# Kernel tuning notes

Measured on AMD Instinct MI355X. Metric: run time of the kernel, lower is better.

Reference implementation:

```python
import jax, jax.numpy as jnp
import numpy as np

N = 100000
E = 1600000
IN_FEATS = 128
HIDDEN = 128
CLASSES = 64


def setup_inputs() -> dict:
    key = jax.random.key(0)
    ks = jax.random.split(key, 8)
    features = jax.random.normal(ks[0], (N, IN_FEATS), dtype=jnp.float32)
    edge_index = jax.random.randint(ks[1], (2, E), 0, N, dtype=jnp.int64 if jax.config.jax_enable_x64 else jnp.int32)
    # Glorot-init weights like PyG's GCNConv.lin, zero bias
    def glorot(k, fan_in, fan_out):
        lim = (6.0 / (fan_in + fan_out)) ** 0.5
        return jax.random.uniform(k, (fan_in, fan_out), dtype=jnp.float32, minval=-lim, maxval=lim)
    return {
        "features": features,
        "edge_index": edge_index,
        "W1": glorot(ks[2], IN_FEATS, HIDDEN), "b1": jnp.zeros((HIDDEN,), jnp.float32),
        "W2": glorot(ks[3], HIDDEN, HIDDEN), "b2": jnp.zeros((HIDDEN,), jnp.float32),
        "W3": glorot(ks[4], HIDDEN, CLASSES), "b3": jnp.zeros((CLASSES,), jnp.float32),
    }


def _gcn_conv(x, W, b, row, col, deg_norm_row, deg_norm_col):
    # x: [N, d_in] -> [N, d_out]. PyG GCNConv: linear first, then normalized aggregation, then bias.
    xw = x @ W                                   # [N, d_out]
    norm = deg_norm_row * deg_norm_col          # [E]
    msg = norm[:, None] * xw[row]               # gather from source nodes
    out = jax.ops.segment_sum(msg, col, num_segments=N)  # scatter-add to dst
    return out + b


def reference(features, edge_index, W1, b1, W2, b2, W3, b3):
    row, col = edge_index[0], edge_index[1]  # source -> target
    # gcn_norm with add_self_loops=False, unit edge weights: deg over dst nodes
    deg = jax.ops.segment_sum(jnp.ones((E,), features.dtype), col, num_segments=N)
    dinv = jnp.where(deg > 0, jax.lax.rsqrt(jnp.maximum(deg, 1.0)), 0.0)
    dn_row, dn_col = dinv[row], dinv[col]
    h = jax.nn.relu(_gcn_conv(features, W1, b1, row, col, dn_row, dn_col))
    h = jax.nn.relu(_gcn_conv(h, W2, b2, row, col, dn_row, dn_col))
    h = jax.nn.relu(_gcn_conv(h, W3, b3, row, col, dn_row, dn_col))
    return h
```

## Files before the change

kernel.cpp:

```cpp
#include <hip/hip_runtime.h>

#define ALIGNUP(x) (((x) + 255) & ~(size_t)255)
#define ABLK 256
#define BSHIFT 9

typedef _Float16 f16x8 __attribute__((ext_vector_type(8)));
typedef float f32x4 __attribute__((ext_vector_type(4)));


__global__ void bucket_hist_kernel(const int* __restrict__ col, unsigned* __restrict__ gHist,
                                   int nE, int chunk) {
    __shared__ unsigned hist[256];
    const int tid = threadIdx.x, blk = blockIdx.x;
    hist[tid] = 0;
    __syncthreads();
    const int e0 = blk * chunk, e1 = min(nE, e0 + chunk);
    for (int e = e0 + tid; e < e1; e += 256)
        atomicAdd(&hist[((unsigned)col[e]) >> BSHIFT], 1u);
    __syncthreads();
    gHist[tid * ABLK + blk] = hist[tid];
}

__global__ void bucket_scan_kernel(unsigned* __restrict__ g) {
    __shared__ unsigned ps[1024];
    const int tid = threadIdx.x;
    const int base = tid * 64;
    unsigned sum = 0;
    for (int k = 0; k < 64; ++k) sum += g[base + k];
    ps[tid] = sum;
    __syncthreads();
    for (int o = 1; o < 1024; o <<= 1) {
        unsigned t = tid >= o ? ps[tid - o] : 0u;
        __syncthreads();
        ps[tid] += t;
        __syncthreads();
    }
    unsigned run = ps[tid] - sum;
    for (int k = 0; k < 64; ++k) {
        unsigned v = g[base + k];
        g[base + k] = run;
        run += v;
    }
}

__global__ void bucket_scatter_kernel(const int* __restrict__ row, const int* __restrict__ col,
                                      const unsigned* __restrict__ gScan,
                                      unsigned* __restrict__ pairs, int nE, int chunk) {
    __shared__ unsigned basec[256];
    const int tid = threadIdx.x, blk = blockIdx.x;
    basec[tid] = gScan[tid * ABLK + blk];
    __syncthreads();
    const int e0 = blk * chunk, e1 = min(nE, e0 + chunk);
    for (int e = e0 + tid; e < e1; e += 256) {
        unsigned d = (unsigned)col[e];
        unsigned pos = atomicAdd(&basec[d >> BSHIFT], 1u);
        pairs[pos] = (((unsigned)row[e]) << BSHIFT) | (d & 511u);
    }
}

__global__ void bucket_sort_kernel(const unsigned* __restrict__ pairs,
                                   const unsigned* __restrict__ gScan,
                                   int* __restrict__ srcs, int* __restrict__ off,
                                   float* __restrict__ dinv, int nN, int nE) {
    __shared__ unsigned cnt[512], sc[512];
    const int tid = threadIdx.x, b = blockIdx.x;
    const unsigned s = gScan[b * ABLK];
    const unsigned t = (b + 1 < 256) ? gScan[(b + 1) * ABLK] : (unsigned)nE;
    cnt[tid] = 0;
    __syncthreads();
    for (unsigned i = s + tid; i < t; i += 512)
        atomicAdd(&cnt[pairs[i] & 511u], 1u);
    __syncthreads();
    const unsigned v = cnt[tid];
    sc[tid] = v;
    __syncthreads();
    for (int o = 1; o < 512; o <<= 1) {
        unsigned q = tid >= o ? sc[tid - o] : 0u;
        __syncthreads();
        sc[tid] += q;
        __syncthreads();
    }
    const unsigned excl = sc[tid] - v;
    const int node = b * 512 + tid;
    if (node < nN) {
        dinv[node] = v > 0 ? rsqrtf((float)v) : 0.f;
        off[node] = (int)(s + excl);
    }
    if (b == 0 && tid == 0) off[nN] = nE;
    sc[tid] = excl;
    __syncthreads();
    for (unsigned i = s + tid; i < t; i += 512) {
        unsigned p = pairs[i];
        unsigned pos = s + atomicAdd(&sc[p & 511u], 1u);
        srcs[pos] = (int)(p >> BSHIFT);
    }
}


template <int DOUT, bool AF32>
__launch_bounds__(256)
__global__ void gemm_mfma(const void* __restrict__ Xv, const float* __restrict__ W,
                          const float* __restrict__ dinv, _Float16* __restrict__ Y, int nrows) {
    constexpr int NTILE = DOUT / 16;
    __shared__ f16x8 Wf[NTILE * 4 * 64];
    const int tid = threadIdx.x;
    for (int idx = tid; idx < 128 * (DOUT / 4); idx += 256) {
        const int kk = idx / (DOUT / 4);
        const int n4 = (idx % (DOUT / 4)) * 4;
        const float4 w = ((const float4*)W)[idx];
        const int fk = kk >> 5, kb = (kk >> 3) & 3, e = kk & 7;
        const float wv[4] = {w.x, w.y, w.z, w.w};
#pragma unroll
        for (int d = 0; d < 4; ++d) {
            const int n = n4 + d;
            const int j = n >> 4;
            const int l = (n & 15) | (kb << 4);
            ((_Float16*)&Wf[(j * 4 + fk) * 64 + l])[e] = (_Float16)wv[d];
        }
    }
    __syncthreads();

    const int lane = tid & 63;
    const int wvid = tid >> 6;
    const int m = lane & 15;
    const int kb = lane >> 4;
    const int nchunks = (nrows + 63) >> 6;

    for (int c = blockIdx.x; c < nchunks; c += gridDim.x) {
        const int r0 = c * 64 + wvid * 16;
        const int arow = min(r0 + m, nrows - 1);
        f16x8 a[4];
        if constexpr (AF32) {
            const float* Xp = (const float*)Xv + (size_t)arow * 128 + kb * 8;
#pragma unroll
            for (int k = 0; k < 4; ++k) {
                const float4 x0 = *(const float4*)(Xp + k * 32);
                const float4 x1 = *(const float4*)(Xp + k * 32 + 4);
                f16x8 t;
                t[0] = (_Float16)x0.x; t[1] = (_Float16)x0.y;
                t[2] = (_Float16)x0.z; t[3] = (_Float16)x0.w;
                t[4] = (_Float16)x1.x; t[5] = (_Float16)x1.y;
                t[6] = (_Float16)x1.z; t[7] = (_Float16)x1.w;
                a[k] = t;
            }
        } else {
            const _Float16* Xp = (const _Float16*)Xv + (size_t)arow * 128 + kb * 8;
#pragma unroll
            for (int k = 0; k < 4; ++k) a[k] = *(const f16x8*)(Xp + k * 32);
        }
        f32x4 acc[NTILE];
#pragma unroll
        for (int j = 0; j < NTILE; ++j) acc[j] = (f32x4){0.f, 0.f, 0.f, 0.f};
#pragma unroll
        for (int k = 0; k < 4; ++k)
#pragma unroll
            for (int j = 0; j < NTILE; ++j)
                acc[j] = __builtin_amdgcn_mfma_f32_16x16x32_f16(
                             a[k], Wf[(j * 4 + k) * 64 + lane], acc[j], 0, 0, 0);
#pragma unroll
        for (int i = 0; i < 4; ++i) {
            const int r = r0 + kb * 4 + i;
            if (r < nrows) {
                const float dv = dinv[r];
#pragma unroll
                for (int j = 0; j < NTILE; ++j)
                    Y[(size_t)r * DOUT + j * 16 + m] = (_Float16)(acc[j][i] * dv);
            }
        }
    }
}


template <int D, typename OT>
__launch_bounds__(256)
__global__ void gather_kernel(const _Float16* __restrict__ XW, const int* __restrict__ off,
                              const int* __restrict__ srcs, const float* __restrict__ dinv,
                              const float* __restrict__ bias, OT* __restrict__ out, int nN) {
    constexpr int G   = D / 8;
    constexpr int EPW = 64 / G;
    const int lane = threadIdx.x & 63;
    const int g    = lane % G;
    const int sub  = lane / G;
    const int wid  = (blockIdx.x * blockDim.x + threadIdx.x) >> 6;
    const int nw   = (gridDim.x * blockDim.x) >> 6;

    for (int v = wid; v < nN; v += nw) {
        const int s1 = off[v + 1];
        int i = off[v] + sub;
        float acc[8];
#pragma unroll
        for (int k = 0; k < 8; ++k) acc[k] = 0.f;
        for (; i + EPW < s1; i += 2 * EPW) {
            int sa = srcs[i], sb = srcs[i + EPW];
            union { uint4 u; _Float16 h[8]; } ca, cb;
            ca.u = ((const uint4*)(XW + (size_t)sa * D))[g];
            cb.u = ((const uint4*)(XW + (size_t)sb * D))[g];
#pragma unroll
            for (int k = 0; k < 8; ++k) acc[k] += (float)ca.h[k];
#pragma unroll
            for (int k = 0; k < 8; ++k) acc[k] += (float)cb.h[k];
        }
        if (i < s1) {
            union { uint4 u; _Float16 h[8]; } cv;
            cv.u = ((const uint4*)(XW + (size_t)srcs[i] * D))[g];
#pragma unroll
            for (int k = 0; k < 8; ++k) acc[k] += (float)cv.h[k];
        }
#pragma unroll
        for (int d = 32; d >= G; d >>= 1)
#pragma unroll
            for (int k = 0; k < 8; ++k) acc[k] += __shfl_down(acc[k], d);
        if (sub == 0) {
            const float dv = dinv[v];
            const float4 b0 = ((const float4*)bias)[g * 2];
            const float4 b1 = ((const float4*)bias)[g * 2 + 1];
            float o[8];
            o[0] = fmaxf(dv * acc[0] + b0.x, 0.f);
            o[1] = fmaxf(dv * acc[1] + b0.y, 0.f);
            o[2] = fmaxf(dv * acc[2] + b0.z, 0.f);
            o[3] = fmaxf(dv * acc[3] + b0.w, 0.f);
            o[4] = fmaxf(dv * acc[4] + b1.x, 0.f);
            o[5] = fmaxf(dv * acc[5] + b1.y, 0.f);
            o[6] = fmaxf(dv * acc[6] + b1.z, 0.f);
            o[7] = fmaxf(dv * acc[7] + b1.w, 0.f);
            if constexpr (sizeof(OT) == 2) {
                union { uint4 u; _Float16 h[8]; } ov;
#pragma unroll
                for (int k = 0; k < 8; ++k) ov.h[k] = (_Float16)o[k];
                *(uint4*)((_Float16*)out + (size_t)v * D + g * 8) = ov.u;
            } else {
                float4 o0 = make_float4(o[0], o[1], o[2], o[3]);
                float4 o1 = make_float4(o[4], o[5], o[6], o[7]);
                float4* op = (float4*)((float*)out + (size_t)v * D + g * 8);
                op[0] = o0;
                op[1] = o1;
            }
        }
    }
}

extern "C" void kernel_launch(void* const* d_in, const int* in_sizes, int n_in,
                              void* d_out, int out_size, void* d_ws, size_t ws_size,
                              hipStream_t stream) {
    const float* feats = (const float*)d_in[0];
    const int*   ei    = (const int*)d_in[1];
    const float* W1    = (const float*)d_in[2];
    const float* b1    = (const float*)d_in[3];
    const float* W2    = (const float*)d_in[4];
    const float* b2    = (const float*)d_in[5];
    const float* W3    = (const float*)d_in[6];
    const float* b3    = (const float*)d_in[7];

    const int N = in_sizes[0] / 128;
    const int E = in_sizes[1] / 2;
    const int* row = ei;
    const int* col = ei + E;

    char* p = (char*)d_ws;
    unsigned* gHist = (unsigned*)p; p += ALIGNUP((size_t)256 * ABLK * 4);
    float*     dinv = (float*)p;    p += ALIGNUP((size_t)N * 4);
    int*       off  = (int*)p;      p += ALIGNUP((size_t)(N + 1) * 4);
    int*       srcs = (int*)p;      p += ALIGNUP((size_t)E * 4);
    _Float16*  bufW = (_Float16*)p; p += ALIGNUP((size_t)N * 128 * 2);
    _Float16*  bufX = (_Float16*)p;
    unsigned* pairs = (unsigned*)bufX;

    const int chunk = (E + ABLK - 1) / ABLK;
    const int NB    = (N + 511) >> BSHIFT;
    bucket_hist_kernel<<<ABLK, 256, 0, stream>>>(col, gHist, E, chunk);
    bucket_scan_kernel<<<1, 1024, 0, stream>>>(gHist);
    bucket_scatter_kernel<<<ABLK, 256, 0, stream>>>(row, col, gHist, pairs, E, chunk);
    bucket_sort_kernel<<<NB, 512, 0, stream>>>(pairs, gHist, srcs, off, dinv, N, E);

    const int NCH = (N + 63) / 64;
    const int GG  = NCH < 800 ? NCH : 800;
    const int GB  = (N + 3) / 4;

    gemm_mfma<128, true><<<GG, 256, 0, stream>>>(feats, W1, dinv, bufW, N);
    gather_kernel<128, _Float16><<<GB, 256, 0, stream>>>(bufW, off, srcs, dinv, b1, bufX, N);
    gemm_mfma<128, false><<<GG, 256, 0, stream>>>(bufX, W2, dinv, bufW, N);
    gather_kernel<128, _Float16><<<GB, 256, 0, stream>>>(bufW, off, srcs, dinv, b2, bufX, N);
    gemm_mfma<64, false><<<GG, 256, 0, stream>>>(bufX, W3, dinv, bufW, N);
    gather_kernel<64, float><<<GB, 256, 0, stream>>>(bufW, off, srcs, dinv, b3,
                                                     (float*)d_out, N);
}
```

Measured before the change: 299.8 us.

## Gather with one 8-lane group per node and split features into column halves

Replaces the wave-per-node gather with a kernel in which each wave handles eight nodes, one 8-lane group per node. Each group loads a batch of source indices cooperatively and broadcasts them with shuffles, so the cross-lane reduction goes away and work per node is finer-grained. The 128-wide layers are now aggregated in two passes over 64-column halves, shrinking the working set of each pass so more of it can stay in cache. The cost is reading the index lists twice per wide layer, launching more kernels, and load imbalance within a wave when node degrees differ.

```diff
diff --git a/kernel.cpp b/kernel.cpp
--- a/kernel.cpp
+++ b/kernel.cpp
@@ -171,49 +171,57 @@
 }
 
 
-template <int D, typename OT>
+template <int DW, int LD, typename OT>
 __launch_bounds__(256)
-__global__ void gather_kernel(const _Float16* __restrict__ XW, const int* __restrict__ off,
-                              const int* __restrict__ srcs, const float* __restrict__ dinv,
-                              const float* __restrict__ bias, OT* __restrict__ out, int nN) {
-    constexpr int G   = D / 8;
-    constexpr int EPW = 64 / G;
+__global__ void gather_grp(const _Float16* __restrict__ XW, const int* __restrict__ off,
+                           const int* __restrict__ srcs, const float* __restrict__ dinv,
+                           const float* __restrict__ bias, OT* __restrict__ out, int nN) {
+    constexpr int G   = DW / 8;
+    constexpr int GPW = 64 / G;
     const int lane = threadIdx.x & 63;
-    const int g    = lane % G;
-    const int sub  = lane / G;
+    const int gl   = lane % G;
+    const int grp  = lane / G;
     const int wid  = (blockIdx.x * blockDim.x + threadIdx.x) >> 6;
     const int nw   = (gridDim.x * blockDim.x) >> 6;
 
-    for (int v = wid; v < nN; v += nw) {
-        const int s1 = off[v + 1];
-        int i = off[v] + sub;
+    for (int v0 = wid * GPW; v0 < nN; v0 += nw * GPW) {
+        const int v   = v0 + grp;
+        const bool act = v < nN;
+        const int s0 = act ? off[v] : 0;
+        const int s1 = act ? off[v + 1] : 0;
         float acc[8];
 #pragma unroll
         for (int k = 0; k < 8; ++k) acc[k] = 0.f;
-        for (; i + EPW < s1; i += 2 * EPW) {
-            int sa = srcs[i], sb = srcs[i + EPW];
-            union { uint4 u; _Float16 h[8]; } ca, cb;
-            ca.u = ((const uint4*)(XW + (size_t)sa * D))[g];
-            cb.u = ((const uint4*)(XW + (size_t)sb * D))[g];
-#pragma unroll
-            for (int k = 0; k < 8; ++k) acc[k] += (float)ca.h[k];
-#pragma unroll
-            for (int k = 0; k < 8; ++k) acc[k] += (float)cb.h[k];
-        }
-        if (i < s1) {
-            union { uint4 u; _Float16 h[8]; } cv;
-            cv.u = ((const uint4*)(XW + (size_t)srcs[i] * D))[g];
-#pragma unroll
-            for (int k = 0; k < 8; ++k) acc[k] += (float)cv.h[k];
-        }
-#pragma unroll
-        for (int d = 32; d >= G; d >>= 1)
-#pragma unroll
-            for (int k = 0; k < 8; ++k) acc[k] += __shfl_down(acc[k], d);
-        if (sub == 0) {
+
+        int base = s0;
+        while (base + G <= s1) {
+            const int myidx = srcs[base + gl];
+#pragma unroll
+            for (int j = 0; j < G; ++j) {
+                const int src = __shfl(myidx, grp * G + j);
+                union { uint4 u; _Float16 h[8]; } cv;
+                cv.u = *(const uint4*)(XW + (size_t)src * LD + gl * 8);
+#pragma unroll
+                for (int k = 0; k < 8; ++k) acc[k] += (float)cv.h[k];
+            }
+            base += G;
+        }
+        if (base < s1) {
+            const int myidx = srcs[min(base + gl, s1 - 1)];
+            const int rem = s1 - base;
+            for (int j = 0; j < rem; ++j) {
+                const int src = __shfl(myidx, grp * G + j);
+                union { uint4 u; _Float16 h[8]; } cv;
+                cv.u = *(const uint4*)(XW + (size_t)src * LD + gl * 8);
+#pragma unroll
+                for (int k = 0; k < 8; ++k) acc[k] += (float)cv.h[k];
+            }
+        }
+
+        if (act) {
             const float dv = dinv[v];
-            const float4 b0 = ((const float4*)bias)[g * 2];
-            const float4 b1 = ((const float4*)bias)[g * 2 + 1];
+            const float4 b0 = ((const float4*)bias)[gl * 2];
+            const float4 b1 = ((const float4*)bias)[gl * 2 + 1];
             float o[8];
             o[0] = fmaxf(dv * acc[0] + b0.x, 0.f);
             o[1] = fmaxf(dv * acc[1] + b0.y, 0.f);
@@ -227,13 +235,11 @@
                 union { uint4 u; _Float16 h[8]; } ov;
 #pragma unroll
                 for (int k = 0; k < 8; ++k) ov.h[k] = (_Float16)o[k];
-                *(uint4*)((_Float16*)out + (size_t)v * D + g * 8) = ov.u;
+                *(uint4*)((_Float16*)out + (size_t)v * LD + gl * 8) = ov.u;
             } else {
-                float4 o0 = make_float4(o[0], o[1], o[2], o[3]);
-                float4 o1 = make_float4(o[4], o[5], o[6], o[7]);
-                float4* op = (float4*)((float*)out + (size_t)v * D + g * 8);
-                op[0] = o0;
-                op[1] = o1;
+                float* op = (float*)out + (size_t)v * LD + gl * 8;
+                *(float4*)op       = make_float4(o[0], o[1], o[2], o[3]);
+                *(float4*)(op + 4) = make_float4(o[4], o[5], o[6], o[7]);
             }
         }
     }
@@ -274,13 +280,19 @@
 
     const int NCH = (N + 63) / 64;
     const int GG  = NCH < 800 ? NCH : 800;
-    const int GB  = (N + 3) / 4;
+    const int GBg = (N + 31) / 32;
 
     gemm_mfma<128, true><<<GG, 256, 0, stream>>>(feats, W1, dinv, bufW, N);
-    gather_kernel<128, _Float16><<<GB, 256, 0, stream>>>(bufW, off, srcs, dinv, b1, bufX, N);
+    gather_grp<64, 128, _Float16><<<GBg, 256, 0, stream>>>(bufW,      off, srcs, dinv,
+                                                           b1,      bufX,      N);
+    gather_grp<64, 128, _Float16><<<GBg, 256, 0, stream>>>(bufW + 64, off, srcs, dinv,
+                                                           b1 + 64, bufX + 64, N);
     gemm_mfma<128, false><<<GG, 256, 0, stream>>>(bufX, W2, dinv, bufW, N);
-    gather_kernel<128, _Float16><<<GB, 256, 0, stream>>>(bufW, off, srcs, dinv, b2, bufX, N);
+    gather_grp<64, 128, _Float16><<<GBg, 256, 0, stream>>>(bufW,      off, srcs, dinv,
+                                                           b2,      bufX,      N);
+    gather_grp<64, 128, _Float16><<<GBg, 256, 0, stream>>>(bufW + 64, off, srcs, dinv,
+                                                           b2 + 64, bufX + 64, N);
     gemm_mfma<64, false><<<GG, 256, 0, stream>>>(bufX, W3, dinv, bufW, N);
-    gather_kernel<64, float><<<GB, 256, 0, stream>>>(bufW, off, srcs, dinv, b3,
-                                                     (float*)d_out, N);
-}
+    gather_grp<64, 64, float><<<GBg, 256, 0, stream>>>(bufW, off, srcs, dinv, b3,
+                                                       (float*)d_out, N);
+}
```

Result: no change. 303.9 us (+1.4%).
